# Kernel tuning notes

Hardware: AMD Instinct MI355X
Metric: run time of the kernel (lower is better)

The kernel has to match this reference:

```python
import jax, jax.numpy as jnp
import numpy as np

ALPHA = 0.2  # LeakyReLU negative slope (args.alpha)


def leaky(v):
    return jax.nn.leaky_relu(v, negative_slope=ALPHA)


def gcn_conv(x, W, b, src, dst, n_nodes, add_loops):
    """PyG GCNConv: out = D^-1/2 (A [+I]) D^-1/2 X W + b, messages src->dst."""
    if add_loops:
        loops = jnp.arange(n_nodes, dtype=src.dtype)
        src = jnp.concatenate([src, loops])
        dst = jnp.concatenate([dst, loops])
    h = x @ W  # [N, d_out]
    deg = jax.ops.segment_sum(jnp.ones_like(dst, dtype=h.dtype), dst, num_segments=n_nodes)
    dis = jnp.where(deg > 0, jax.lax.rsqrt(jnp.maximum(deg, 1e-12)), 0.0).astype(h.dtype)
    norm = dis[src] * dis[dst]  # [E]
    out = jax.ops.segment_sum(h[src] * norm[:, None], dst, num_segments=n_nodes)
    return out + b


def setup_inputs() -> dict:
    key = jax.random.key(0)
    ks = jax.random.split(key, 16)
    N, M, F, H, C, E = 100000, 1000, 128, 64, 2, 1600000

    x = jax.random.normal(ks[0], (N, F), dtype=jnp.float32)
    edge_index = jax.random.randint(ks[1], (2, E), 0, N, dtype=jnp.int64)
    meta_x = jax.random.normal(ks[2], (M, F), dtype=jnp.float32)

    # meta graph: one edge per data node into a meta node (offset by N), plus self loops
    src_d = jnp.arange(N, dtype=jnp.int64)
    dst_d = jax.random.randint(ks[3], (N,), 0, M, dtype=jnp.int64) + N
    loops = jnp.arange(N + M, dtype=jnp.int64)
    meta_edge_index = jnp.stack([jnp.concatenate([src_d, loops]),
                                 jnp.concatenate([dst_d, loops])])  # [2, 201000]

    s = 0.05
    return {
        "x": x, "edge_index": edge_index,
        "meta_x": meta_x, "meta_edge_index": meta_edge_index,
        "W_lin": jax.random.normal(ks[4], (F, H), dtype=jnp.float32) * s,
        "b_lin": jnp.zeros((H,), jnp.float32),
        "W_mlin": jax.random.normal(ks[5], (F, H), dtype=jnp.float32) * s,
        "b_mlin": jnp.zeros((H,), jnp.float32),
        "W0": jax.random.normal(ks[6], (H, H), dtype=jnp.float32) * s,
        "b0": jnp.zeros((H,), jnp.float32),
        "W1": jax.random.normal(ks[7], (H, H), dtype=jnp.float32) * s,
        "b1": jnp.zeros((H,), jnp.float32),
        "Wm": jax.random.normal(ks[8], (H, H), dtype=jnp.float32) * s,
        "bm": jnp.zeros((H,), jnp.float32),
        "Wc": jax.random.normal(ks[9], (H, C), dtype=jnp.float32) * s,
        "bc": jnp.zeros((C,), jnp.float32),
    }


def reference(x, edge_index, meta_x, meta_edge_index,
              W_lin, b_lin, W_mlin, b_mlin,
              W0, b0, W1, b1, Wm, bm, Wc, bc):
    N = x.shape[0]
    M = meta_x.shape[0]
    src, dst = edge_index[0], edge_index[1]
    msrc, mdst = meta_edge_index[0], meta_edge_index[1]

    # input projections (eval mode: dropout is identity)
    h = leaky(x @ W_lin + b_lin)            # [N, H]
    mh = leaky(meta_x @ W_mlin + b_mlin)    # [M, H]

    # stacked GCN layers on the data graph
    h = leaky(gcn_conv(h, W0, b0, src, dst, N, add_loops=True))
    h = leaky(gcn_conv(h, W1, b1, src, dst, N, add_loops=True))

    # meta-graph fusion: concat data and meta nodes, one GCN pass
    z = jnp.concatenate([h, mh], axis=0)    # [N+M, H]
    z = leaky(gcn_conv(z, Wm, bm, msrc, mdst, N + M, add_loops=False))

    logits = z @ Wc + bc                    # [N+M, C]
    return jax.nn.log_softmax(logits, axis=1)
```

## Files before the change

### kernel.cpp

```cpp
#include <hip/hip_runtime.h>
#include <cstddef>

static constexpr float ALPHA = 0.2f;
static constexpr int H = 64;
static constexpr int NBMAX = 1024;

typedef __attribute__((ext_vector_type(8))) short short8;
typedef __attribute__((ext_vector_type(4))) float floatx4;

__device__ __forceinline__ float lrelu(float v) { return v >= 0.0f ? v : ALPHA * v; }

__device__ __forceinline__ float b2f(unsigned short u)
{
    union { unsigned int i; float f; } x;
    x.i = ((unsigned int)u) << 16;
    return x.f;
}

__device__ __forceinline__ unsigned short f2b(float f)
{
    union { float f; unsigned int i; } x;
    x.f = f;
    unsigned int r = x.i + 0x7fffu + ((x.i >> 16) & 1u);
    return (unsigned short)(r >> 16);
}

template <int K, bool AF32, bool BIAS, bool ACT, bool SCALE>
__global__ __launch_bounds__(256) void mfma_gemm(
    const void* __restrict__ in_v, const float* __restrict__ W,
    const float* __restrict__ bias, const float* __restrict__ scl,
    unsigned short* __restrict__ out, int rows)
{
    constexpr int S = K / 32;
    __shared__ short8 WL[4 * S * 64];

    for (int f = threadIdx.x; f < 4 * S * 64; f += 256) {
        int c = f / (S * 64);
        int rem = f % (S * 64);
        int s = rem / 64;
        int l = rem % 64;
        short8 frag;
        #pragma unroll
        for (int j = 0; j < 8; ++j) {
            int k = s * 32 + (l >> 4) * 8 + j;
            int col = c * 16 + (l & 15);
            frag[j] = (short)f2b(W[k * H + col]);
        }
        WL[f] = frag;
    }
    __syncthreads();

    const int l = threadIdx.x & 63;
    const int wv = threadIdx.x >> 6;
    const int rowBase = blockIdx.x * 64 + wv * 16;
    if (rowBase >= rows) return;
    const int arow = min(rowBase + (l & 15), rows - 1);

    floatx4 acc0 = {0.f, 0.f, 0.f, 0.f};
    floatx4 acc1 = {0.f, 0.f, 0.f, 0.f};
    floatx4 acc2 = {0.f, 0.f, 0.f, 0.f};
    floatx4 acc3 = {0.f, 0.f, 0.f, 0.f};

    #pragma unroll
    for (int s = 0; s < S; ++s) {
        short8 a;
        if (AF32) {
            const float* ap = (const float*)in_v + (size_t)arow * K + s * 32 + (l >> 4) * 8;
            float4 f0 = *(const float4*)(ap + 0);
            float4 f1 = *(const float4*)(ap + 4);
            a[0] = (short)f2b(f0.x); a[1] = (short)f2b(f0.y);
            a[2] = (short)f2b(f0.z); a[3] = (short)f2b(f0.w);
            a[4] = (short)f2b(f1.x); a[5] = (short)f2b(f1.y);
            a[6] = (short)f2b(f1.z); a[7] = (short)f2b(f1.w);
        } else {
            a = *(const short8*)((const unsigned short*)in_v + (size_t)arow * K + s * 32 + (l >> 4) * 8);
        }
        acc0 = __builtin_amdgcn_mfma_f32_16x16x32_bf16(a, WL[(0 * S + s) * 64 + l], acc0, 0, 0, 0);
        acc1 = __builtin_amdgcn_mfma_f32_16x16x32_bf16(a, WL[(1 * S + s) * 64 + l], acc1, 0, 0, 0);
        acc2 = __builtin_amdgcn_mfma_f32_16x16x32_bf16(a, WL[(2 * S + s) * 64 + l], acc2, 0, 0, 0);
        acc3 = __builtin_amdgcn_mfma_f32_16x16x32_bf16(a, WL[(3 * S + s) * 64 + l], acc3, 0, 0, 0);
    }

    #pragma unroll
    for (int j = 0; j < 4; ++j) {
        int row = rowBase + (l >> 4) * 4 + j;
        if (row >= rows) continue;
        unsigned short* orow = out + (size_t)row * H;
        float sc = SCALE ? scl[row] : 1.0f;
        float v;
        int col = l & 15;
        v = acc0[j] + (BIAS ? bias[col] : 0.f);      if (ACT) v = lrelu(v); orow[col]      = f2b(v * sc);
        v = acc1[j] + (BIAS ? bias[col + 16] : 0.f); if (ACT) v = lrelu(v); orow[col + 16] = f2b(v * sc);
        v = acc2[j] + (BIAS ? bias[col + 32] : 0.f); if (ACT) v = lrelu(v); orow[col + 32] = f2b(v * sc);
        v = acc3[j] + (BIAS ? bias[col + 48] : 0.f); if (ACT) v = lrelu(v); orow[col + 48] = f2b(v * sc);
    }
}


__global__ __launch_bounds__(256) void zero_i(int* __restrict__ p, int n)
{
    int i = blockIdx.x * 256 + threadIdx.x;
    if (i < n) p[i] = 0;
}

__global__ __launch_bounds__(256) void bhist(const int* __restrict__ dst, int* __restrict__ gbh,
                                             int nE, int nb)
{
    __shared__ int lh[NBMAX];
    for (int i = threadIdx.x; i < nb; i += 256) lh[i] = 0;
    __syncthreads();
    for (int i = blockIdx.x * 256 + threadIdx.x; i < nE; i += 256 * gridDim.x)
        atomicAdd(&lh[dst[i] >> 7], 1);
    __syncthreads();
    for (int b = threadIdx.x; b < nb; b += 256) {
        int v = lh[b];
        if (v) atomicAdd(&gbh[b], v);
    }
}

__global__ __launch_bounds__(256) void bscan(const int* __restrict__ gbh, int* __restrict__ goff,
                                             int* __restrict__ gcur, int nb)
{
    __shared__ int sp[256];
    int t = threadIdx.x;
    int base = t * 4;
    int a0 = base + 0 < nb ? gbh[base + 0] : 0;
    int a1 = base + 1 < nb ? gbh[base + 1] : 0;
    int a2 = base + 2 < nb ? gbh[base + 2] : 0;
    int a3 = base + 3 < nb ? gbh[base + 3] : 0;
    int s = a0 + a1 + a2 + a3;
    sp[t] = s;
    __syncthreads();
    for (int o = 1; o < 256; o <<= 1) {
        int y = (t >= o) ? sp[t - o] : 0;
        __syncthreads();
        sp[t] += y;
        __syncthreads();
    }
    int e = sp[t] - s;
    if (base + 0 < nb) { goff[base + 0] = e;                gcur[base + 0] = e; }
    if (base + 1 < nb) { goff[base + 1] = e + a0;           gcur[base + 1] = e + a0; }
    if (base + 2 < nb) { goff[base + 2] = e + a0 + a1;      gcur[base + 2] = e + a0 + a1; }
    if (base + 3 < nb) { goff[base + 3] = e + a0 + a1 + a2; gcur[base + 3] = e + a0 + a1 + a2; }
}

__global__ __launch_bounds__(256) void bfill(const int* __restrict__ src, const int* __restrict__ dst,
                                             int* __restrict__ gcur, int* __restrict__ ebuf,
                                             int nE, int nb, int tile)
{
    __shared__ int lh[NBMAX];
    __shared__ int lst[NBMAX];
    const int t = threadIdx.x;
    const int base = blockIdx.x * tile;
    const int nT = min(tile, nE - base);

    for (int i = t; i < nb; i += 256) lh[i] = 0;
    __syncthreads();
    for (int i = t; i < nT; i += 256) atomicAdd(&lh[dst[base + i] >> 7], 1);
    __syncthreads();
    for (int b = t; b < nb; b += 256) {
        int k = lh[b];
        lst[b] = k ? atomicAdd(&gcur[b], k) : 0;
    }
    __syncthreads();
    for (int i = t; i < nT; i += 256) {
        int d = dst[base + i];
        int b = d >> 7;
        int pos = atomicAdd(&lst[b], 1);
        ebuf[pos] = ((d & 127) << 17) | src[base + i];
    }
}

__global__ __launch_bounds__(256) void local_csr(const int* __restrict__ ebuf, const int* __restrict__ goff,
                                                 const int* __restrict__ gbh, int* __restrict__ esrc,
                                                 int* __restrict__ rs, int* __restrict__ cnt,
                                                 float* __restrict__ dis, int n, int selfadd)
{
    __shared__ int lcnt[128];
    __shared__ int lrs[128];
    __shared__ int lcur[128];
    const int b = blockIdx.x;
    const int t = threadIdx.x;
    const int off = goff[b];
    const int k = gbh[b];

    if (t < 128) lcnt[t] = 0;
    __syncthreads();
    for (int i = t; i < k; i += 256) atomicAdd(&lcnt[ebuf[off + i] >> 17], 1);
    __syncthreads();
    if (t < 128) lrs[t] = lcnt[t];
    __syncthreads();
    for (int o = 1; o < 128; o <<= 1) {
        int y = (t < 128 && t >= o) ? lrs[t - o] : 0;
        __syncthreads();
        if (t < 128) lrs[t] += y;
        __syncthreads();
    }
    if (t < 128) lcur[t] = lrs[t] - lcnt[t];
    __syncthreads();
    for (int i = t; i < k; i += 256) {
        int v = ebuf[off + i];
        int dL = v >> 17;
        int pos = atomicAdd(&lcur[dL], 1);
        esrc[off + pos] = v & 0x1FFFF;
    }
    int node = b * 128 + t;
    if (t < 128 && node < n) {
        int c = lcnt[t];
        rs[node] = off + (lrs[t] - c);
        cnt[node] = c;
        int dt = c + selfadd;
        dis[node] = dt > 0 ? rsqrtf((float)dt) : 0.0f;
    }
}

template <bool SELF, bool FINAL>
__global__ __launch_bounds__(256) void gather16(const unsigned short* __restrict__ h,
                                                const int* __restrict__ esrc,
                                                const int* __restrict__ rs, const int* __restrict__ cnt,
                                                const float* __restrict__ dis, const float* __restrict__ bias,
                                                unsigned short* __restrict__ out,
                                                const float* __restrict__ Wc, const float* __restrict__ bc,
                                                float* __restrict__ fout, int n)
{
    int d = blockIdx.x * 16 + (threadIdx.x >> 4);
    if (d >= n) return;
    const int l = threadIdx.x & 15;
    const int beg = rs[d];
    const int c = cnt[d];
    const float dd = dis[d];

    float ax0 = 0.f, ay0 = 0.f, az0 = 0.f, aw0 = 0.f;
    float ax1 = 0.f, ay1 = 0.f, az1 = 0.f, aw1 = 0.f;
    int i = 0;
    for (; i + 2 <= c; i += 2) {
        int s0 = esrc[beg + i], s1 = esrc[beg + i + 1];
        ushort4 v0 = *(const ushort4*)(h + (size_t)s0 * H + l * 4);
        ushort4 v1 = *(const ushort4*)(h + (size_t)s1 * H + l * 4);
        ax0 += b2f(v0.x); ay0 += b2f(v0.y); az0 += b2f(v0.z); aw0 += b2f(v0.w);
        ax1 += b2f(v1.x); ay1 += b2f(v1.y); az1 += b2f(v1.z); aw1 += b2f(v1.w);
    }
    if (i < c) {
        int s = esrc[beg + i];
        ushort4 v = *(const ushort4*)(h + (size_t)s * H + l * 4);
        ax0 += b2f(v.x); ay0 += b2f(v.y); az0 += b2f(v.z); aw0 += b2f(v.w);
    }
    if (SELF) {
        ushort4 v = *(const ushort4*)(h + (size_t)d * H + l * 4);
        ax0 += b2f(v.x); ay0 += b2f(v.y); az0 += b2f(v.z); aw0 += b2f(v.w);
    }

    float rx = (ax0 + ax1) * dd, ry = (ay0 + ay1) * dd, rz = (az0 + az1) * dd, rw = (aw0 + aw1) * dd;
    float4 bb = *(const float4*)(bias + l * 4);
    rx = lrelu(rx + bb.x); ry = lrelu(ry + bb.y); rz = lrelu(rz + bb.z); rw = lrelu(rw + bb.w);

    if (FINAL) {
        int f = l * 4;
        float p0 = rx * Wc[(f + 0) * 2] + ry * Wc[(f + 1) * 2] + rz * Wc[(f + 2) * 2] + rw * Wc[(f + 3) * 2];
        float p1 = rx * Wc[(f + 0) * 2 + 1] + ry * Wc[(f + 1) * 2 + 1] + rz * Wc[(f + 2) * 2 + 1] + rw * Wc[(f + 3) * 2 + 1];
        #pragma unroll
        for (int o = 8; o; o >>= 1) {
            p0 += __shfl_xor(p0, o);
            p1 += __shfl_xor(p1, o);
        }
        if (l == 0) {
            float l0 = p0 + bc[0], l1 = p1 + bc[1];
            float m = fmaxf(l0, l1);
            float lse = m + logf(expf(l0 - m) + expf(l1 - m));
            fout[(size_t)d * 2 + 0] = l0 - lse;
            fout[(size_t)d * 2 + 1] = l1 - lse;
        }
    } else {
        ushort4 o;
        o.x = f2b(rx); o.y = f2b(ry); o.z = f2b(rz); o.w = f2b(rw);
        *(ushort4*)(out + (size_t)d * H + l * 4) = o;
    }
}

extern "C" void kernel_launch(void* const* d_in, const int* in_sizes, int n_in,
                              void* d_out, int out_size, void* d_ws, size_t ws_size,
                              hipStream_t stream)
{
    const float* x      = (const float*)d_in[0];
    const int*   ei     = (const int*)d_in[1];
    const float* mx     = (const float*)d_in[2];
    const int*   mei    = (const int*)d_in[3];
    const float* W_lin  = (const float*)d_in[4];
    const float* b_lin  = (const float*)d_in[5];
    const float* W_mlin = (const float*)d_in[6];
    const float* b_mlin = (const float*)d_in[7];
    const float* W0     = (const float*)d_in[8];
    const float* b0     = (const float*)d_in[9];
    const float* W1     = (const float*)d_in[10];
    const float* b1     = (const float*)d_in[11];
    const float* Wm     = (const float*)d_in[12];
    const float* bm     = (const float*)d_in[13];
    const float* Wc     = (const float*)d_in[14];
    const float* bc     = (const float*)d_in[15];

    const int F  = 128;
    const int N  = in_sizes[0] / F;
    const int E  = in_sizes[1] / 2;
    const int M  = in_sizes[2] / F;
    const int Em = in_sizes[3] / 2;
    const int NM = N + M;
    const int* src  = ei;
    const int* dstp = ei + E;
    const int* msrc = mei;
    const int* mdst = mei + Em;
    const int Emax = E > Em ? E : Em;

    unsigned short* hb0 = (unsigned short*)d_ws;
    unsigned short* hb1 = hb0 + (size_t)NM * H;
    float* disD = (float*)(hb1 + (size_t)NM * H);
    float* disM = disD + NM;
    int*   cntD = (int*)(disM + NM);
    int*   rsD  = cntD + NM;
    int*   cntM = rsD + NM;
    int*   rsM  = cntM + NM;
    int*   esrcD = rsM + NM;
    int*   esrcM = esrcD + E;
    int*   ebuf  = esrcM + Em;
    int*   gbh  = ebuf + Emax;
    int*   goff = gbh + NBMAX;
    int*   gcur = goff + NBMAX;

    const int nbD = (N + 127) / 128;
    const int nbM = (NM + 127) / 128;
    const int tileD = 6144;
    const int tileM = 1024;

    mfma_gemm<128, true, true, true, false><<<(N + 63) / 64, 256, 0, stream>>>(x, W_lin, b_lin, nullptr, hb0, N);
    mfma_gemm<128, true, true, true, false><<<(M + 63) / 64, 256, 0, stream>>>(mx, W_mlin, b_mlin, nullptr, hb0 + (size_t)N * H, M);

    zero_i<<<(NBMAX + 255) / 256, 256, 0, stream>>>(gbh, NBMAX);
    bhist<<<min(256, (E + 255) / 256), 256, 0, stream>>>(dstp, gbh, E, nbD);
    bscan<<<1, 256, 0, stream>>>(gbh, goff, gcur, nbD);
    bfill<<<(E + tileD - 1) / tileD, 256, 0, stream>>>(src, dstp, gcur, ebuf, E, nbD, tileD);
    local_csr<<<nbD, 256, 0, stream>>>(ebuf, goff, gbh, esrcD, rsD, cntD, disD, N, 1);

    zero_i<<<(NBMAX + 255) / 256, 256, 0, stream>>>(gbh, NBMAX);
    bhist<<<min(256, (Em + 255) / 256), 256, 0, stream>>>(mdst, gbh, Em, nbM);
    bscan<<<1, 256, 0, stream>>>(gbh, goff, gcur, nbM);
    bfill<<<(Em + tileM - 1) / tileM, 256, 0, stream>>>(msrc, mdst, gcur, ebuf, Em, nbM, tileM);
    local_csr<<<nbM, 256, 0, stream>>>(ebuf, goff, gbh, esrcM, rsM, cntM, disM, NM, 0);

    mfma_gemm<64, false, false, false, true><<<(N + 63) / 64, 256, 0, stream>>>(hb0, W0, nullptr, disD, hb1, N);
    gather16<true, false><<<(N + 15) / 16, 256, 0, stream>>>(hb1, esrcD, rsD, cntD, disD, b0, hb0, nullptr, nullptr, nullptr, N);

    mfma_gemm<64, false, false, false, true><<<(N + 63) / 64, 256, 0, stream>>>(hb0, W1, nullptr, disD, hb1, N);
    gather16<true, false><<<(N + 15) / 16, 256, 0, stream>>>(hb1, esrcD, rsD, cntD, disD, b1, hb0, nullptr, nullptr, nullptr, N);

    mfma_gemm<64, false, false, false, true><<<(NM + 63) / 64, 256, 0, stream>>>(hb0, Wm, nullptr, disM, hb1, NM);

    gather16<false, true><<<(NM + 15) / 16, 256, 0, stream>>>(hb1, esrcM, rsM, cntM, disM, bm, nullptr, Wc, bc, (float*)d_out, NM);
}
```

Before: 292.1 us.

## Merge data and meta CSR builds into one pass and widen gather to wave-per-node

The separate bucket-sort CSR pipelines for the data graph and the meta graph are merged into one histogram, scan, fill and local-CSR pass over concatenated edges. The fill kernel now uses a fixed 2048-edge tile held in registers. The gather kernel assigns a full 64-lane wavefront per destination node, with four edge groups reduced by cross-lane shuffles, to get more memory parallelism per node. This removes several kernel launches and raises in-flight loads, at the cost of more shuffles and three of four lane groups sitting idle during the store.

New measurement: 288.0 us. About the same (-1.4%).

```diff
diff --git a/kernel.cpp b/kernel.cpp
--- a/kernel.cpp
+++ b/kernel.cpp
@@ -3,7 +3,8 @@
 
 static constexpr float ALPHA = 0.2f;
 static constexpr int H = 64;
-static constexpr int NBMAX = 1024;
+static constexpr int NBMAX = 2048;
+static constexpr int BTILE = 2048;
 
 typedef __attribute__((ext_vector_type(8))) short short8;
 typedef __attribute__((ext_vector_type(4))) float floatx4;
@@ -103,16 +104,18 @@
     if (i < n) p[i] = 0;
 }
 
-__global__ __launch_bounds__(256) void bhist(const int* __restrict__ dst, int* __restrict__ gbh,
-                                             int nE, int nb)
+__global__ __launch_bounds__(256) void bhist(const int* __restrict__ dstD, const int* __restrict__ dstM,
+                                             int* __restrict__ gbh, int E, int Et, int nbD, int nbT)
 {
     __shared__ int lh[NBMAX];
-    for (int i = threadIdx.x; i < nb; i += 256) lh[i] = 0;
-    __syncthreads();
-    for (int i = blockIdx.x * 256 + threadIdx.x; i < nE; i += 256 * gridDim.x)
-        atomicAdd(&lh[dst[i] >> 7], 1);
-    __syncthreads();
-    for (int b = threadIdx.x; b < nb; b += 256) {
+    for (int i = threadIdx.x; i < nbT; i += 256) lh[i] = 0;
+    __syncthreads();
+    for (int j = blockIdx.x * 256 + threadIdx.x; j < Et; j += 256 * gridDim.x) {
+        int b = (j < E) ? (dstD[j] >> 7) : (nbD + (dstM[j - E] >> 7));
+        atomicAdd(&lh[b], 1);
+    }
+    __syncthreads();
+    for (int b = threadIdx.x; b < nbT; b += 256) {
         int v = lh[b];
         if (v) atomicAdd(&gbh[b], v);
     }
@@ -123,12 +126,14 @@
 {
     __shared__ int sp[256];
     int t = threadIdx.x;
-    int base = t * 4;
-    int a0 = base + 0 < nb ? gbh[base + 0] : 0;
-    int a1 = base + 1 < nb ? gbh[base + 1] : 0;
-    int a2 = base + 2 < nb ? gbh[base + 2] : 0;
-    int a3 = base + 3 < nb ? gbh[base + 3] : 0;
-    int s = a0 + a1 + a2 + a3;
+    int base = t * 8;
+    int a[8];
+    int s = 0;
+    #pragma unroll
+    for (int u = 0; u < 8; ++u) {
+        a[u] = (base + u < nb) ? gbh[base + u] : 0;
+        s += a[u];
+    }
     sp[t] = s;
     __syncthreads();
     for (int o = 1; o < 256; o <<= 1) {
@@ -138,43 +143,59 @@
         __syncthreads();
     }
     int e = sp[t] - s;
-    if (base + 0 < nb) { goff[base + 0] = e;                gcur[base + 0] = e; }
-    if (base + 1 < nb) { goff[base + 1] = e + a0;           gcur[base + 1] = e + a0; }
-    if (base + 2 < nb) { goff[base + 2] = e + a0 + a1;      gcur[base + 2] = e + a0 + a1; }
-    if (base + 3 < nb) { goff[base + 3] = e + a0 + a1 + a2; gcur[base + 3] = e + a0 + a1 + a2; }
-}
-
-__global__ __launch_bounds__(256) void bfill(const int* __restrict__ src, const int* __restrict__ dst,
+    #pragma unroll
+    for (int u = 0; u < 8; ++u) {
+        if (base + u < nb) { goff[base + u] = e; gcur[base + u] = e; }
+        e += a[u];
+    }
+}
+
+__global__ __launch_bounds__(256) void bfill(const int* __restrict__ srcD, const int* __restrict__ dstD,
+                                             const int* __restrict__ srcM, const int* __restrict__ dstM,
                                              int* __restrict__ gcur, int* __restrict__ ebuf,
-                                             int nE, int nb, int tile)
+                                             int E, int Et, int nbD, int nbT)
 {
     __shared__ int lh[NBMAX];
     __shared__ int lst[NBMAX];
     const int t = threadIdx.x;
-    const int base = blockIdx.x * tile;
-    const int nT = min(tile, nE - base);
-
-    for (int i = t; i < nb; i += 256) lh[i] = 0;
-    __syncthreads();
-    for (int i = t; i < nT; i += 256) atomicAdd(&lh[dst[base + i] >> 7], 1);
-    __syncthreads();
-    for (int b = t; b < nb; b += 256) {
+    const int base = blockIdx.x * BTILE;
+
+    for (int i = t; i < nbT; i += 256) lh[i] = 0;
+    __syncthreads();
+
+    int bb[8], pk[8];
+    #pragma unroll
+    for (int u = 0; u < 8; ++u) {
+        int j = base + u * 256 + t;
+        if (j < Et) {
+            int d, sv;
+            if (j < E) { d = dstD[j]; sv = srcD[j]; bb[u] = d >> 7; }
+            else       { d = dstM[j - E]; sv = srcM[j - E]; bb[u] = nbD + (d >> 7); }
+            pk[u] = ((d & 127) << 17) | sv;
+            atomicAdd(&lh[bb[u]], 1);
+        } else bb[u] = -1;
+    }
+    __syncthreads();
+
+    for (int b = t; b < nbT; b += 256) {
         int k = lh[b];
         lst[b] = k ? atomicAdd(&gcur[b], k) : 0;
     }
     __syncthreads();
-    for (int i = t; i < nT; i += 256) {
-        int d = dst[base + i];
-        int b = d >> 7;
-        int pos = atomicAdd(&lst[b], 1);
-        ebuf[pos] = ((d & 127) << 17) | src[base + i];
+
+    #pragma unroll
+    for (int u = 0; u < 8; ++u) {
+        if (bb[u] >= 0) {
+            int pos = atomicAdd(&lst[bb[u]], 1);
+            ebuf[pos] = pk[u];
+        }
     }
 }
 
 __global__ __launch_bounds__(256) void local_csr(const int* __restrict__ ebuf, const int* __restrict__ goff,
                                                  const int* __restrict__ gbh, int* __restrict__ esrc,
                                                  int* __restrict__ rs, int* __restrict__ cnt,
-                                                 float* __restrict__ dis, int n, int selfadd)
+                                                 float* __restrict__ dis, int nbD, int N, int NM)
 {
     __shared__ int lcnt[128];
     __shared__ int lrs[128];
@@ -183,6 +204,7 @@
     const int t = threadIdx.x;
     const int off = goff[b];
     const int k = gbh[b];
+    const bool isData = b < nbD;
 
     if (t < 128) lcnt[t] = 0;
     __syncthreads();
@@ -204,18 +226,22 @@
         int pos = atomicAdd(&lcur[dL], 1);
         esrc[off + pos] = v & 0x1FFFF;
     }
-    int node = b * 128 + t;
-    if (t < 128 && node < n) {
-        int c = lcnt[t];
-        rs[node] = off + (lrs[t] - c);
-        cnt[node] = c;
-        int dt = c + selfadd;
-        dis[node] = dt > 0 ? rsqrtf((float)dt) : 0.0f;
+    if (t < 128) {
+        int local = isData ? b * 128 + t : (b - nbD) * 128 + t;
+        int lim = isData ? N : NM;
+        if (local < lim) {
+            int slot = isData ? local : N + local;
+            int c = lcnt[t];
+            rs[slot] = off + (lrs[t] - c);
+            cnt[slot] = c;
+            int dt = c + (isData ? 1 : 0);
+            dis[slot] = dt > 0 ? rsqrtf((float)dt) : 0.0f;
+        }
     }
 }
 
 template <bool SELF, bool FINAL>
-__global__ __launch_bounds__(256) void gather16(const unsigned short* __restrict__ h,
+__global__ __launch_bounds__(256) void gather_w(const unsigned short* __restrict__ h,
                                                 const int* __restrict__ esrc,
                                                 const int* __restrict__ rs, const int* __restrict__ cnt,
                                                 const float* __restrict__ dis, const float* __restrict__ bias,
@@ -223,39 +249,47 @@
                                                 const float* __restrict__ Wc, const float* __restrict__ bc,
                                                 float* __restrict__ fout, int n)
 {
-    int d = blockIdx.x * 16 + (threadIdx.x >> 4);
+    int d = blockIdx.x * 4 + (threadIdx.x >> 6);
     if (d >= n) return;
-    const int l = threadIdx.x & 15;
+    const int l = threadIdx.x & 63;
+    const int g = l >> 4;
+    const int fq = l & 15;
     const int beg = rs[d];
     const int c = cnt[d];
     const float dd = dis[d];
 
     float ax0 = 0.f, ay0 = 0.f, az0 = 0.f, aw0 = 0.f;
     float ax1 = 0.f, ay1 = 0.f, az1 = 0.f, aw1 = 0.f;
-    int i = 0;
-    for (; i + 2 <= c; i += 2) {
-        int s0 = esrc[beg + i], s1 = esrc[beg + i + 1];
-        ushort4 v0 = *(const ushort4*)(h + (size_t)s0 * H + l * 4);
-        ushort4 v1 = *(const ushort4*)(h + (size_t)s1 * H + l * 4);
+    int i = g;
+    for (; i + 4 < c; i += 8) {
+        int s0 = esrc[beg + i], s1 = esrc[beg + i + 4];
+        ushort4 v0 = *(const ushort4*)(h + (size_t)s0 * H + fq * 4);
+        ushort4 v1 = *(const ushort4*)(h + (size_t)s1 * H + fq * 4);
         ax0 += b2f(v0.x); ay0 += b2f(v0.y); az0 += b2f(v0.z); aw0 += b2f(v0.w);
         ax1 += b2f(v1.x); ay1 += b2f(v1.y); az1 += b2f(v1.z); aw1 += b2f(v1.w);
     }
     if (i < c) {
         int s = esrc[beg + i];
-        ushort4 v = *(const ushort4*)(h + (size_t)s * H + l * 4);
+        ushort4 v = *(const ushort4*)(h + (size_t)s * H + fq * 4);
         ax0 += b2f(v.x); ay0 += b2f(v.y); az0 += b2f(v.z); aw0 += b2f(v.w);
     }
+
+    float rx = ax0 + ax1, ry = ay0 + ay1, rz = az0 + az1, rw = aw0 + aw1;
+    rx += __shfl_xor(rx, 16); rx += __shfl_xor(rx, 32);
+    ry += __shfl_xor(ry, 16); ry += __shfl_xor(ry, 32);
+    rz += __shfl_xor(rz, 16); rz += __shfl_xor(rz, 32);
+    rw += __shfl_xor(rw, 16); rw += __shfl_xor(rw, 32);
+
     if (SELF) {
-        ushort4 v = *(const ushort4*)(h + (size_t)d * H + l * 4);
-        ax0 += b2f(v.x); ay0 += b2f(v.y); az0 += b2f(v.z); aw0 += b2f(v.w);
-    }
-
-    float rx = (ax0 + ax1) * dd, ry = (ay0 + ay1) * dd, rz = (az0 + az1) * dd, rw = (aw0 + aw1) * dd;
-    float4 bb = *(const float4*)(bias + l * 4);
-    rx = lrelu(rx + bb.x); ry = lrelu(ry + bb.y); rz = lrelu(rz + bb.z); rw = lrelu(rw + bb.w);
+        ushort4 v = *(const ushort4*)(h + (size_t)d * H + fq * 4);
+        rx += b2f(v.x); ry += b2f(v.y); rz += b2f(v.z); rw += b2f(v.w);
+    }
+    float4 bb = *(const float4*)(bias + fq * 4);
+    rx = lrelu(rx * dd + bb.x); ry = lrelu(ry * dd + bb.y);
+    rz = lrelu(rz * dd + bb.z); rw = lrelu(rw * dd + bb.w);
 
     if (FINAL) {
-        int f = l * 4;
+        int f = fq * 4;
         float p0 = rx * Wc[(f + 0) * 2] + ry * Wc[(f + 1) * 2] + rz * Wc[(f + 2) * 2] + rw * Wc[(f + 3) * 2];
         float p1 = rx * Wc[(f + 0) * 2 + 1] + ry * Wc[(f + 1) * 2 + 1] + rz * Wc[(f + 2) * 2 + 1] + rw * Wc[(f + 3) * 2 + 1];
         #pragma unroll
@@ -271,9 +305,11 @@
             fout[(size_t)d * 2 + 1] = l1 - lse;
         }
     } else {
-        ushort4 o;
-        o.x = f2b(rx); o.y = f2b(ry); o.z = f2b(rz); o.w = f2b(rw);
-        *(ushort4*)(out + (size_t)d * H + l * 4) = o;
+        if (g == 0) {
+            ushort4 o;
+            o.x = f2b(rx); o.y = f2b(ry); o.z = f2b(rz); o.w = f2b(rw);
+            *(ushort4*)(out + (size_t)d * H + fq * 4) = o;
+        }
     }
 }
 
@@ -304,54 +340,43 @@
     const int M  = in_sizes[2] / F;
     const int Em = in_sizes[3] / 2;
     const int NM = N + M;
+    const int Et = E + Em;
     const int* src  = ei;
     const int* dstp = ei + E;
     const int* msrc = mei;
     const int* mdst = mei + Em;
-    const int Emax = E > Em ? E : Em;
 
     unsigned short* hb0 = (unsigned short*)d_ws;
     unsigned short* hb1 = hb0 + (size_t)NM * H;
-    float* disD = (float*)(hb1 + (size_t)NM * H);
-    float* disM = disD + NM;
-    int*   cntD = (int*)(disM + NM);
-    int*   rsD  = cntD + NM;
-    int*   cntM = rsD + NM;
-    int*   rsM  = cntM + NM;
-    int*   esrcD = rsM + NM;
-    int*   esrcM = esrcD + E;
-    int*   ebuf  = esrcM + Em;
-    int*   gbh  = ebuf + Emax;
+    float* disV = (float*)(hb1 + (size_t)NM * H);
+    int*   cntV = (int*)(disV + (N + NM));
+    int*   rsV  = cntV + (N + NM);
+    int*   esrcA = rsV + (N + NM);
+    int*   ebuf  = esrcA + Et;
+    int*   gbh  = ebuf + Et;
     int*   goff = gbh + NBMAX;
     int*   gcur = goff + NBMAX;
 
     const int nbD = (N + 127) / 128;
     const int nbM = (NM + 127) / 128;
-    const int tileD = 6144;
-    const int tileM = 1024;
+    const int nbT = nbD + nbM;
 
     mfma_gemm<128, true, true, true, false><<<(N + 63) / 64, 256, 0, stream>>>(x, W_lin, b_lin, nullptr, hb0, N);
     mfma_gemm<128, true, true, true, false><<<(M + 63) / 64, 256, 0, stream>>>(mx, W_mlin, b_mlin, nullptr, hb0 + (size_t)N * H, M);
 
     zero_i<<<(NBMAX + 255) / 256, 256, 0, stream>>>(gbh, NBMAX);
-    bhist<<<min(256, (E + 255) / 256), 256, 0, stream>>>(dstp, gbh, E, nbD);
-    bscan<<<1, 256, 0, stream>>>(gbh, goff, gcur, nbD);
-    bfill<<<(E + tileD - 1) / tileD, 256, 0, stream>>>(src, dstp, gcur, ebuf, E, nbD, tileD);
-    local_csr<<<nbD, 256, 0, stream>>>(ebuf, goff, gbh, esrcD, rsD, cntD, disD, N, 1);
-
-    zero_i<<<(NBMAX + 255) / 256, 256, 0, stream>>>(gbh, NBMAX);
-    bhist<<<min(256, (Em + 255) / 256), 256, 0, stream>>>(mdst, gbh, Em, nbM);
-    bscan<<<1, 256, 0, stream>>>(gbh, goff, gcur, nbM);
-    bfill<<<(Em + tileM - 1) / tileM, 256, 0, stream>>>(msrc, mdst, gcur, ebuf, Em, nbM, tileM);
-    local_csr<<<nbM, 256, 0, stream>>>(ebuf, goff, gbh, esrcM, rsM, cntM, disM, NM, 0);
-
-    mfma_gemm<64, false, false, false, true><<<(N + 63) / 64, 256, 0, stream>>>(hb0, W0, nullptr, disD, hb1, N);
-    gather16<true, false><<<(N + 15) / 16, 256, 0, stream>>>(hb1, esrcD, rsD, cntD, disD, b0, hb0, nullptr, nullptr, nullptr, N);
-
-    mfma_gemm<64, false, false, false, true><<<(N + 63) / 64, 256, 0, stream>>>(hb0, W1, nullptr, disD, hb1, N);
-    gather16<true, false><<<(N + 15) / 16, 256, 0, stream>>>(hb1, esrcD, rsD, cntD, disD, b1, hb0, nullptr, nullptr, nullptr, N);
-
-    mfma_gemm<64, false, false, false, true><<<(NM + 63) / 64, 256, 0, stream>>>(hb0, Wm, nullptr, disM, hb1, NM);
-
-    gather16<false, true><<<(NM + 15) / 16, 256, 0, stream>>>(hb1, esrcM, rsM, cntM, disM, bm, nullptr, Wc, bc, (float*)d_out, NM);
-}
+    bhist<<<256, 256, 0, stream>>>(dstp, mdst, gbh, E, Et, nbD, nbT);
+    bscan<<<1, 256, 0, stream>>>(gbh, goff, gcur, nbT);
+    bfill<<<(Et + BTILE - 1) / BTILE, 256, 0, stream>>>(src, dstp, msrc, mdst, gcur, ebuf, E, Et, nbD, nbT);
+    local_csr<<<nbT, 256, 0, stream>>>(ebuf, goff, gbh, esrcA, rsV, cntV, disV, nbD, N, NM);
+
+    mfma_gemm<64, false, false, false, true><<<(N + 63) / 64, 256, 0, stream>>>(hb0, W0, nullptr, disV, hb1, N);
+    gather_w<true, false><<<(N + 3) / 4, 256, 0, stream>>>(hb1, esrcA, rsV, cntV, disV, b0, hb0, nullptr, nullptr, nullptr, N);
+
+    mfma_gemm<64, false, false, false, true><<<(N + 63) / 64, 256, 0, stream>>>(hb0, W1, nullptr, disV, hb1, N);
+    gather_w<true, false><<<(N + 3) / 4, 256, 0, stream>>>(hb1, esrcA, rsV, cntV, disV, b1, hb0, nullptr, nullptr, nullptr, N);
+
+    mfma_gemm<64, false, false, false, true><<<(NM + 63) / 64, 256, 0, stream>>>(hb0, Wm, nullptr, disV + N, hb1, NM);
+
+    gather_w<false, true><<<(NM + 3) / 4, 256, 0, stream>>>(hb1, esrcA, rsV + N, cntV + N, disV + N, bm, nullptr, Wc, bc, (float*)d_out, NM);
+}
```
